# Optimization experiments

Measured on AMD Instinct MI355X. Metric: run time of the kernel, lower is better.

## Reference

```python
import jax, jax.numpy as jnp
import numpy as np

B, T, D, H = 4, 2048, 384, 6
HD = D // H  # 64
HALF = HD // 2


def setup_inputs() -> dict:
    key = jax.random.key(0)
    k0, k1, k2 = jax.random.split(key, 3)
    x = jax.random.normal(k0, (B, T, D), jnp.float32)
    attn_bias = jnp.zeros((1, 1, T, T), jnp.float32)  # additive SDPA bias
    # standard RoPE tables: [T, HD/2]
    inv_freq = 1.0 / (10000.0 ** (np.arange(HALF, dtype=np.float32) / HALF))
    ang = np.arange(T, dtype=np.float32)[:, None] * inv_freq[None, :]
    cos = jnp.asarray(np.cos(ang), jnp.float32)
    sin = jnp.asarray(np.sin(ang), jnp.float32)
    w_qkv = jax.random.normal(k1, (D, 3 * D), jnp.float32) * (D ** -0.5)
    w_proj = jax.random.normal(k2, (D, D), jnp.float32) * (D ** -0.5)
    return {"x": x, "attn_bias": attn_bias, "cos": cos, "sin": sin,
            "w_qkv": w_qkv, "w_proj": w_proj}


def _apply_rope(x, cos, sin):
    # x: [b, h, t, hd]; cos/sin: [t, hd/2] -> rotate-half RoPE
    half = x.shape[-1] // 2
    x1, x2 = x[..., :half], x[..., half:]
    c = cos[None, None, :, :]
    s = sin[None, None, :, :]
    return jnp.concatenate([x1 * c - x2 * s, x2 * c + x1 * s], axis=-1)


def reference(x, attn_bias, cos, sin, w_qkv, w_proj):
    b, t, _ = x.shape
    qkv = (x @ w_qkv).reshape(b, t, 3, H, HD)  # fused QKV projection
    q = jnp.transpose(qkv[:, :, 0], (0, 2, 1, 3))  # [b,h,t,hd]
    k = jnp.transpose(qkv[:, :, 1], (0, 2, 1, 3))
    v = jnp.transpose(qkv[:, :, 2], (0, 2, 1, 3))
    q = _apply_rope(q, cos, sin)
    k = _apply_rope(k, cos, sin)
    scale = 1.0 / jnp.sqrt(jnp.asarray(HD, x.dtype))
    scores = jnp.einsum("bhqd,bhkd->bhqk", q, k) * scale + attn_bias
    attn = jax.nn.softmax(scores, axis=-1)
    out = jnp.einsum("bhqk,bhkd->bhqd", attn, v)
    out = jnp.transpose(out, (0, 2, 1, 3)).reshape(b, t, H * HD)
    return out @ w_proj
```

## Files before the change

### kernel.cpp

```cpp
#include <hip/hip_runtime.h>
#include <hip/hip_bf16.h>

#define BB   4
#define TT   2048
#define DDIM 384
#define HH   6
#define HD   64
#define BT   (BB*TT)
#define QKVC (3*DDIM)

typedef __attribute__((ext_vector_type(4))) short short4v;
typedef __attribute__((ext_vector_type(8))) short short8v;
typedef __attribute__((ext_vector_type(4))) float float4v;
typedef unsigned short u16;

static __device__ __forceinline__ u16 f2bu(float f) {
    __hip_bfloat16 h = __float2bfloat16(f);
    return __builtin_bit_cast(u16, h);
}

static __device__ __forceinline__ short8v ld_frag(const u16* p) {
    short4v a = *(const short4v*)p;
    short4v b = *(const short4v*)(p + 4);
    return __builtin_shufflevector(a, b, 0, 1, 2, 3, 4, 5, 6, 7);
}

static __device__ __forceinline__ void st8(u16* p, uint4 v) {
    *(uint2*)p       = make_uint2(v.x, v.y);
    *(uint2*)(p + 4) = make_uint2(v.z, v.w);
}

#define MFMA16(a, b, c) __builtin_amdgcn_mfma_f32_16x16x32_bf16((a), (b), (c), 0, 0, 0)

__global__ __launch_bounds__(256) void prep_kernel(
    const float* __restrict__ wqkv, const float* __restrict__ wproj,
    const float* __restrict__ x,
    u16* __restrict__ wqkvT, u16* __restrict__ wprojT, u16* __restrict__ xb)
{
    const int bid = blockIdx.x;
    const int t = threadIdx.x;
    if (bid >= 144) {
        size_t base = (size_t)(bid - 144) * 4096 + (size_t)t * 16;
        const float* gp = x + base;
        __align__(16) u16 tmp[16];
        #pragma unroll
        for (int u = 0; u < 4; ++u) {
            float4 v = *(const float4*)(gp + 4 * u);
            tmp[4 * u + 0] = f2bu(v.x); tmp[4 * u + 1] = f2bu(v.y);
            tmp[4 * u + 2] = f2bu(v.z); tmp[4 * u + 3] = f2bu(v.w);
        }
        *(uint4*)(xb + base)     = *(const uint4*)tmp;
        *(uint4*)(xb + base + 8) = *(const uint4*)(tmp + 8);
        return;
    }
    const float* in; u16* out; int K, C, c0, k0;
    if (bid < 108) { in = wqkv;  out = wqkvT;  K = DDIM; C = QKVC;
                     c0 = (bid % 18) * 64; k0 = (bid / 18) * 64; }
    else           { int b2 = bid - 108; in = wproj; out = wprojT; K = DDIM; C = DDIM;
                     c0 = (b2 % 6) * 64; k0 = (b2 / 6) * 64; }
    __shared__ float tr[64][65];
    {
        int kr = t >> 2, cb = (t & 3) * 16;
        const float* gp = in + (size_t)(k0 + kr) * C + c0 + cb;
        #pragma unroll
        for (int u = 0; u < 4; ++u) {
            float4 v = *(const float4*)(gp + 4 * u);
            tr[cb + 4 * u + 0][kr] = v.x;
            tr[cb + 4 * u + 1][kr] = v.y;
            tr[cb + 4 * u + 2][kr] = v.z;
            tr[cb + 4 * u + 3][kr] = v.w;
        }
    }
    __syncthreads();
    {
        int c = t >> 2, kb = (t & 3) * 16;
        __align__(16) u16 tmp[16];
        #pragma unroll
        for (int u = 0; u < 16; ++u) tmp[u] = f2bu(tr[c][kb + u]);
        u16* op = out + (size_t)(c0 + c) * K + k0 + kb;
        *(uint4*)op       = *(const uint4*)tmp;
        *(uint4*)(op + 8) = *(const uint4*)(tmp + 8);
    }
}

__global__ __launch_bounds__(256) void qkv_rope_kernel(
    const u16* __restrict__ xb, const u16* __restrict__ wt,
    const float* __restrict__ cs, const float* __restrict__ sn,
    u16* __restrict__ qb, u16* __restrict__ kb, u16* __restrict__ vtb)
{
    __shared__ __align__(16) u16 xs[2][64][68];
    __shared__ __align__(16) u16 ws[2][64][68];
    const int t = threadIdx.x;
    const int wv = t >> 6, lane = t & 63, quad = lane >> 4, lo = lane & 15;
    const int r0 = blockIdx.y * 64;
    const int c0 = blockIdx.x * 64;
    const int sr = t >> 3, sd = (t & 7) * 8;

    st8(&xs[0][sr][sd],      *(const uint4*)(xb + (size_t)(r0 + sr) * DDIM + sd));
    st8(&xs[0][sr + 32][sd], *(const uint4*)(xb + (size_t)(r0 + sr + 32) * DDIM + sd));
    st8(&ws[0][sr][sd],      *(const uint4*)(wt + (size_t)(c0 + sr) * DDIM + sd));
    st8(&ws[0][sr + 32][sd], *(const uint4*)(wt + (size_t)(c0 + sr + 32) * DDIM + sd));
    __syncthreads();

    float4v acc[4] = {};
    for (int kk = 0; kk < 6; ++kk) {
        const int cur = kk & 1, nxt = cur ^ 1;
        const int kkn = (kk < 5 ? kk + 1 : 5) * 64;
        uint4 xp0 = *(const uint4*)(xb + (size_t)(r0 + sr) * DDIM + kkn + sd);
        uint4 xp1 = *(const uint4*)(xb + (size_t)(r0 + sr + 32) * DDIM + kkn + sd);
        uint4 wp0 = *(const uint4*)(wt + (size_t)(c0 + sr) * DDIM + kkn + sd);
        uint4 wp1 = *(const uint4*)(wt + (size_t)(c0 + sr + 32) * DDIM + kkn + sd);

        #pragma unroll
        for (int kf = 0; kf < 2; ++kf) {
            short8v a = ld_frag(&xs[cur][16 * wv + lo][kf * 32 + quad * 8]);
            #pragma unroll
            for (int nt = 0; nt < 4; ++nt) {
                short8v b = ld_frag(&ws[cur][nt * 16 + lo][kf * 32 + quad * 8]);
                acc[nt] = MFMA16(a, b, acc[nt]);
            }
        }
        st8(&xs[nxt][sr][sd], xp0);
        st8(&xs[nxt][sr + 32][sd], xp1);
        st8(&ws[nxt][sr][sd], wp0);
        st8(&ws[nxt][sr + 32][sd], wp1);
        __syncthreads();
    }

    const int sec = blockIdx.x / 6;
    const int h   = blockIdx.x % 6;
    const int rbase = r0 + 16 * wv + 4 * quad;
    const int bidx  = r0 >> 11;
    const int tbase = rbase & (TT - 1);

    if (sec == 2) {
        #pragma unroll
        for (int nt = 0; nt < 4; ++nt) {
            int d = nt * 16 + lo;
            unsigned a0 = f2bu(acc[nt][0]) | ((unsigned)f2bu(acc[nt][1]) << 16);
            unsigned a1 = f2bu(acc[nt][2]) | ((unsigned)f2bu(acc[nt][3]) << 16);
            u16* gp = vtb + ((size_t)(bidx * HH + h) * HD + d) * TT + tbase;
            *(uint2*)gp = make_uint2(a0, a1);
        }
    } else {
        u16* dst = (sec == 0) ? qb : kb;
        #pragma unroll
        for (int np = 0; np < 2; ++np) {
            #pragma unroll
            for (int r = 0; r < 4; ++r) {
                int tpos = tbase + r;
                int ci = np * 16 + lo;
                float cv = cs[tpos * 32 + ci];
                float sv = sn[tpos * 32 + ci];
                float x1 = acc[np][r], x2 = acc[np + 2][r];
                u16* gp = dst + ((size_t)(bidx * HH + h) * TT + tpos) * HD;
                gp[ci]      = f2bu(x1 * cv - x2 * sv);
                gp[ci + 32] = f2bu(x2 * cv + x1 * sv);
            }
        }
    }
}

__global__ __launch_bounds__(256, 3) void attn_kernel(
    const u16* __restrict__ qb, const u16* __restrict__ kb, const u16* __restrict__ vtb,
    const float* __restrict__ bias, u16* __restrict__ ob)
{
    __shared__ __align__(16) u16 ks[2][64][68];
    __shared__ __align__(16) u16 vt[2][64][68];
    __shared__ __align__(16) u16 ps[4][16][72];

    const int t = threadIdx.x;
    const int wv = t >> 6, lane = t & 63, quad = lane >> 4, lo = lane & 15;
    const int bh = blockIdx.x;
    const int b = bh / HH, h = bh % HH;
    const int q0 = blockIdx.y * 64;
    const int qrow = q0 + 16 * wv + lo;

    const u16* qbase = qb + ((size_t)bh * TT + qrow) * HD + quad * 8;
    short8v aq0 = __builtin_bit_cast(short8v, *(const uint4*)qbase);
    short8v aq1 = __builtin_bit_cast(short8v, *(const uint4*)(qbase + 32));

    const int sr = t >> 3, sd = (t & 7) * 8;
    const u16* kbbase = kb + (size_t)bh * TT * HD;
    const u16* vtbase = vtb + (size_t)bh * HD * TT;
    const float* brow = bias + (size_t)qrow * TT + 4 * quad;

    st8(&ks[0][sr][sd],      *(const uint4*)(kbbase + (size_t)sr * HD + sd));
    st8(&ks[0][sr + 32][sd], *(const uint4*)(kbbase + (size_t)(sr + 32) * HD + sd));
    st8(&vt[0][sr][sd],      *(const uint4*)(vtbase + (size_t)sr * TT + sd));
    st8(&vt[0][sr + 32][sd], *(const uint4*)(vtbase + (size_t)(sr + 32) * TT + sd));
    float4 bcur[4];
    #pragma unroll
    for (int nt = 0; nt < 4; ++nt) bcur[nt] = *(const float4*)(brow + nt * 16);
    __syncthreads();

    float4v oacc[4] = {};
    float lacc[4] = {0.f, 0.f, 0.f, 0.f};

    for (int kt = 0; kt < TT / 64; ++kt) {
        const int cur = kt & 1, nxt = cur ^ 1;
        const int kn = (kt < 31 ? kt + 1 : 31) * 64;

        uint4 kp0 = *(const uint4*)(kbbase + (size_t)(kn + sr) * HD + sd);
        uint4 kp1 = *(const uint4*)(kbbase + (size_t)(kn + sr + 32) * HD + sd);
        uint4 vp0 = *(const uint4*)(vtbase + (size_t)sr * TT + kn + sd);
        uint4 vp1 = *(const uint4*)(vtbase + (size_t)(sr + 32) * TT + kn + sd);
        float4 bnxt[4];
        #pragma unroll
        for (int nt = 0; nt < 4; ++nt) bnxt[nt] = *(const float4*)(brow + kn + nt * 16);

        float4v s[4] = {};
        #pragma unroll
        for (int kf = 0; kf < 2; ++kf) {
            #pragma unroll
            for (int nt = 0; nt < 4; ++nt) {
                short8v kfr = ld_frag(&ks[cur][nt * 16 + lo][kf * 32 + quad * 8]);
                s[nt] = MFMA16(kfr, (kf ? aq1 : aq0), s[nt]);
            }
        }

        #pragma unroll
        for (int nt = 0; nt < 4; ++nt) {
            float p0 = __expf(fmaf(s[nt][0], 0.125f, bcur[nt].x));
            float p1 = __expf(fmaf(s[nt][1], 0.125f, bcur[nt].y));
            float p2 = __expf(fmaf(s[nt][2], 0.125f, bcur[nt].z));
            float p3 = __expf(fmaf(s[nt][3], 0.125f, bcur[nt].w));
            lacc[nt] += (p0 + p1) + (p2 + p3);
            short4v pv = { (short)f2bu(p0), (short)f2bu(p1),
                           (short)f2bu(p2), (short)f2bu(p3) };
            *(short4v*)&ps[wv][lo][nt * 16 + 4 * quad] = pv;
        }

        #pragma unroll
        for (int kf = 0; kf < 2; ++kf) {
            short8v ap = __builtin_bit_cast(short8v,
                *(const uint4*)&ps[wv][lo][kf * 32 + quad * 8]);
            #pragma unroll
            for (int dt = 0; dt < 4; ++dt) {
                short8v bv = ld_frag(&vt[cur][dt * 16 + lo][kf * 32 + quad * 8]);
                oacc[dt] = MFMA16(ap, bv, oacc[dt]);
            }
        }

        st8(&ks[nxt][sr][sd], kp0);
        st8(&ks[nxt][sr + 32][sd], kp1);
        st8(&vt[nxt][sr][sd], vp0);
        st8(&vt[nxt][sr + 32][sd], vp1);
        #pragma unroll
        for (int nt = 0; nt < 4; ++nt) bcur[nt] = bnxt[nt];
        __syncthreads();
    }

    float l = (lacc[0] + lacc[1]) + (lacc[2] + lacc[3]);
    l += __shfl_xor(l, 16);
    l += __shfl_xor(l, 32);
    #pragma unroll
    for (int r = 0; r < 4; ++r) {
        float lr = __shfl(l, 4 * quad + r);
        float inv = 1.f / lr;
        u16* gp = ob + ((size_t)b * TT + q0 + 16 * wv + 4 * quad + r) * DDIM + h * HD + lo;
        #pragma unroll
        for (int dt = 0; dt < 4; ++dt)
            gp[dt * 16] = f2bu(oacc[dt][r] * inv);
    }
}

__global__ __launch_bounds__(256) void proj_kernel(
    const u16* __restrict__ o, const u16* __restrict__ wt, float* __restrict__ out)
{
    __shared__ __align__(16) u16 os[2][64][68];
    __shared__ __align__(16) u16 ws[2][64][68];
    const int t = threadIdx.x;
    const int wv = t >> 6, lane = t & 63, quad = lane >> 4, lo = lane & 15;
    const int r0 = blockIdx.y * 64, c0 = blockIdx.x * 64;
    const int sr = t >> 3, sd = (t & 7) * 8;

    st8(&os[0][sr][sd],      *(const uint4*)(o + (size_t)(r0 + sr) * DDIM + sd));
    st8(&os[0][sr + 32][sd], *(const uint4*)(o + (size_t)(r0 + sr + 32) * DDIM + sd));
    st8(&ws[0][sr][sd],      *(const uint4*)(wt + (size_t)(c0 + sr) * DDIM + sd));
    st8(&ws[0][sr + 32][sd], *(const uint4*)(wt + (size_t)(c0 + sr + 32) * DDIM + sd));
    __syncthreads();

    float4v acc[4] = {};
    for (int kk = 0; kk < 6; ++kk) {
        const int cur = kk & 1, nxt = cur ^ 1;
        const int kkn = (kk < 5 ? kk + 1 : 5) * 64;
        uint4 op0 = *(const uint4*)(o + (size_t)(r0 + sr) * DDIM + kkn + sd);
        uint4 op1 = *(const uint4*)(o + (size_t)(r0 + sr + 32) * DDIM + kkn + sd);
        uint4 wp0 = *(const uint4*)(wt + (size_t)(c0 + sr) * DDIM + kkn + sd);
        uint4 wp1 = *(const uint4*)(wt + (size_t)(c0 + sr + 32) * DDIM + kkn + sd);

        #pragma unroll
        for (int kf = 0; kf < 2; ++kf) {
            short8v a = ld_frag(&os[cur][16 * wv + lo][kf * 32 + quad * 8]);
            #pragma unroll
            for (int nt = 0; nt < 4; ++nt) {
                short8v bfr = ld_frag(&ws[cur][nt * 16 + lo][kf * 32 + quad * 8]);
                acc[nt] = MFMA16(a, bfr, acc[nt]);
            }
        }
        st8(&os[nxt][sr][sd], op0);
        st8(&os[nxt][sr + 32][sd], op1);
        st8(&ws[nxt][sr][sd], wp0);
        st8(&ws[nxt][sr + 32][sd], wp1);
        __syncthreads();
    }
    #pragma unroll
    for (int r = 0; r < 4; ++r) {
        float* gp = out + (size_t)(r0 + 16 * wv + 4 * quad + r) * DDIM + c0;
        #pragma unroll
        for (int nt = 0; nt < 4; ++nt)
            gp[nt * 16 + lo] = acc[nt][r];
    }
}

extern "C" void kernel_launch(void* const* d_in, const int* in_sizes, int n_in,
                              void* d_out, int out_size, void* d_ws, size_t ws_size,
                              hipStream_t stream) {
    const float* x     = (const float*)d_in[0];
    const float* bias  = (const float*)d_in[1];
    const float* cs    = (const float*)d_in[2];
    const float* sn    = (const float*)d_in[3];
    const float* wqkv  = (const float*)d_in[4];
    const float* wproj = (const float*)d_in[5];
    float* out = (float*)d_out;

    u16* wqkvT  = (u16*)d_ws;
    u16* wprojT = wqkvT + (size_t)QKVC * DDIM;
    u16* qb     = wprojT + (size_t)DDIM * DDIM;
    u16* kb     = qb + (size_t)BB * HH * TT * HD;
    u16* vtb    = kb + (size_t)BB * HH * TT * HD;
    u16* ob     = vtb + (size_t)BB * HH * TT * HD;
    u16* xb     = ob + (size_t)BT * DDIM;

    prep_kernel<<<dim3(144 + BT * DDIM / 4096), 256, 0, stream>>>(
        wqkv, wproj, x, wqkvT, wprojT, xb);
    qkv_rope_kernel<<<dim3(QKVC / 64, BT / 64), 256, 0, stream>>>(
        xb, wqkvT, cs, sn, qb, kb, vtb);
    attn_kernel<<<dim3(BB * HH, TT / 64), 256, 0, stream>>>(qb, kb, vtb, bias, ob);
    proj_kernel<<<dim3(DDIM / 64, BT / 64), 256, 0, stream>>>(ob, wprojT, out);
}
```

Before: 178.6 us.

## Split attention keys across two blocks with merge kernel and MFMA row sums

The attention kernel now splits the key sequence into two halves along a new grid dimension, doubling the block count. Each block writes unnormalized fp32 partial outputs and row sums, and a new merge kernel combines and normalizes them into bf16. Shared memory drops from double to single buffering, launch bounds request 6 blocks per SM, and row sums now come from an MFMA against a ones vector instead of scalar adds. The cost is extra fp32 partial-output traffic, one more launch, and an extra sync per tile. Skipping max-subtraction in the split is consistent with the original kernel.

```diff
diff --git a/kernel.cpp b/kernel.cpp
--- a/kernel.cpp
+++ b/kernel.cpp
@@ -161,12 +161,12 @@
     }
 }
 
-__global__ __launch_bounds__(256, 3) void attn_kernel(
+__global__ __launch_bounds__(256, 6) void attn_kernel(
     const u16* __restrict__ qb, const u16* __restrict__ kb, const u16* __restrict__ vtb,
-    const float* __restrict__ bias, u16* __restrict__ ob)
-{
-    __shared__ __align__(16) u16 ks[2][64][68];
-    __shared__ __align__(16) u16 vt[2][64][68];
+    const float* __restrict__ bias, float* __restrict__ opart, float* __restrict__ lws)
+{
+    __shared__ __align__(16) u16 ks[64][68];
+    __shared__ __align__(16) u16 vt[64][68];
     __shared__ __align__(16) u16 ps[4][16][72];
 
     const int t = threadIdx.x;
@@ -174,6 +174,8 @@
     const int bh = blockIdx.x;
     const int b = bh / HH, h = bh % HH;
     const int q0 = blockIdx.y * 64;
+    const int half = blockIdx.z;
+    const int kbase0 = half * (TT / 2);
     const int qrow = q0 + 16 * wv + lo;
 
     const u16* qbase = qb + ((size_t)bh * TT + qrow) * HD + quad * 8;
@@ -181,40 +183,46 @@
     short8v aq1 = __builtin_bit_cast(short8v, *(const uint4*)(qbase + 32));
 
     const int sr = t >> 3, sd = (t & 7) * 8;
-    const u16* kbbase = kb + (size_t)bh * TT * HD;
-    const u16* vtbase = vtb + (size_t)bh * HD * TT;
-    const float* brow = bias + (size_t)qrow * TT + 4 * quad;
-
-    st8(&ks[0][sr][sd],      *(const uint4*)(kbbase + (size_t)sr * HD + sd));
-    st8(&ks[0][sr + 32][sd], *(const uint4*)(kbbase + (size_t)(sr + 32) * HD + sd));
-    st8(&vt[0][sr][sd],      *(const uint4*)(vtbase + (size_t)sr * TT + sd));
-    st8(&vt[0][sr + 32][sd], *(const uint4*)(vtbase + (size_t)(sr + 32) * TT + sd));
-    float4 bcur[4];
-    #pragma unroll
-    for (int nt = 0; nt < 4; ++nt) bcur[nt] = *(const float4*)(brow + nt * 16);
-    __syncthreads();
+    const u16* kbbase = kb + ((size_t)bh * TT + kbase0) * HD;
+    const u16* vtbase = vtb + (size_t)bh * HD * TT + kbase0;
+    const float* brow = bias + (size_t)qrow * TT + kbase0 + 4 * quad;
+
+    const short8v bones = { 0x3F80, 0x3F80, 0x3F80, 0x3F80,
+                            0x3F80, 0x3F80, 0x3F80, 0x3F80 };
+
+    uint4 kp0 = *(const uint4*)(kbbase + (size_t)sr * HD + sd);
+    uint4 kp1 = *(const uint4*)(kbbase + (size_t)(sr + 32) * HD + sd);
+    uint4 vp0 = *(const uint4*)(vtbase + (size_t)sr * TT + sd);
+    uint4 vp1 = *(const uint4*)(vtbase + (size_t)(sr + 32) * TT + sd);
 
     float4v oacc[4] = {};
-    float lacc[4] = {0.f, 0.f, 0.f, 0.f};
-
-    for (int kt = 0; kt < TT / 64; ++kt) {
-        const int cur = kt & 1, nxt = cur ^ 1;
-        const int kn = (kt < 31 ? kt + 1 : 31) * 64;
-
-        uint4 kp0 = *(const uint4*)(kbbase + (size_t)(kn + sr) * HD + sd);
-        uint4 kp1 = *(const uint4*)(kbbase + (size_t)(kn + sr + 32) * HD + sd);
-        uint4 vp0 = *(const uint4*)(vtbase + (size_t)sr * TT + kn + sd);
-        uint4 vp1 = *(const uint4*)(vtbase + (size_t)(sr + 32) * TT + kn + sd);
-        float4 bnxt[4];
-        #pragma unroll
-        for (int nt = 0; nt < 4; ++nt) bnxt[nt] = *(const float4*)(brow + kn + nt * 16);
+    float4v lsum = {};
+
+    for (int kt = 0; kt < TT / 128; ++kt) {
+        __syncthreads();
+        st8(&ks[sr][sd], kp0);
+        st8(&ks[sr + 32][sd], kp1);
+        st8(&vt[sr][sd], vp0);
+        st8(&vt[sr + 32][sd], vp1);
+        __syncthreads();
+
+        const int kn = (kt < TT / 128 - 1 ? kt + 1 : kt) * 64;
+        kp0 = *(const uint4*)(kbbase + (size_t)(kn + sr) * HD + sd);
+        kp1 = *(const uint4*)(kbbase + (size_t)(kn + sr + 32) * HD + sd);
+        vp0 = *(const uint4*)(vtbase + (size_t)sr * TT + kn + sd);
+        vp1 = *(const uint4*)(vtbase + (size_t)(sr + 32) * TT + kn + sd);
+
+        float4 bcur[4];
+        #pragma unroll
+        for (int nt = 0; nt < 4; ++nt)
+            bcur[nt] = *(const float4*)(brow + kt * 64 + nt * 16);
 
         float4v s[4] = {};
         #pragma unroll
         for (int kf = 0; kf < 2; ++kf) {
             #pragma unroll
             for (int nt = 0; nt < 4; ++nt) {
-                short8v kfr = ld_frag(&ks[cur][nt * 16 + lo][kf * 32 + quad * 8]);
+                short8v kfr = ld_frag(&ks[nt * 16 + lo][kf * 32 + quad * 8]);
                 s[nt] = MFMA16(kfr, (kf ? aq1 : aq0), s[nt]);
             }
         }
@@ -225,7 +233,6 @@
             float p1 = __expf(fmaf(s[nt][1], 0.125f, bcur[nt].y));
             float p2 = __expf(fmaf(s[nt][2], 0.125f, bcur[nt].z));
             float p3 = __expf(fmaf(s[nt][3], 0.125f, bcur[nt].w));
-            lacc[nt] += (p0 + p1) + (p2 + p3);
             short4v pv = { (short)f2bu(p0), (short)f2bu(p1),
                            (short)f2bu(p2), (short)f2bu(p3) };
             *(short4v*)&ps[wv][lo][nt * 16 + 4 * quad] = pv;
@@ -235,34 +242,44 @@
         for (int kf = 0; kf < 2; ++kf) {
             short8v ap = __builtin_bit_cast(short8v,
                 *(const uint4*)&ps[wv][lo][kf * 32 + quad * 8]);
+            lsum = MFMA16(ap, bones, lsum);
             #pragma unroll
             for (int dt = 0; dt < 4; ++dt) {
-                short8v bv = ld_frag(&vt[cur][dt * 16 + lo][kf * 32 + quad * 8]);
+                short8v bv = ld_frag(&vt[dt * 16 + lo][kf * 32 + quad * 8]);
                 oacc[dt] = MFMA16(ap, bv, oacc[dt]);
             }
         }
-
-        st8(&ks[nxt][sr][sd], kp0);
-        st8(&ks[nxt][sr + 32][sd], kp1);
-        st8(&vt[nxt][sr][sd], vp0);
-        st8(&vt[nxt][sr + 32][sd], vp1);
-        #pragma unroll
-        for (int nt = 0; nt < 4; ++nt) bcur[nt] = bnxt[nt];
-        __syncthreads();
-    }
-
-    float l = (lacc[0] + lacc[1]) + (lacc[2] + lacc[3]);
-    l += __shfl_xor(l, 16);
-    l += __shfl_xor(l, 32);
+    }
+
     #pragma unroll
     for (int r = 0; r < 4; ++r) {
-        float lr = __shfl(l, 4 * quad + r);
-        float inv = 1.f / lr;
-        u16* gp = ob + ((size_t)b * TT + q0 + 16 * wv + 4 * quad + r) * DDIM + h * HD + lo;
+        int row = q0 + 16 * wv + 4 * quad + r;
+        if (lo == 0)
+            lws[((size_t)half * (BB * HH) + bh) * TT + row] = lsum[r];
+        float* gp = opart + (((size_t)half * BB + b) * TT + row) * DDIM + h * HD + lo;
         #pragma unroll
         for (int dt = 0; dt < 4; ++dt)
-            gp[dt * 16] = f2bu(oacc[dt][r] * inv);
-    }
+            gp[dt * 16] = oacc[dt][r];
+    }
+}
+
+__global__ __launch_bounds__(256) void merge_kernel(
+    const float* __restrict__ opart, const float* __restrict__ lws,
+    u16* __restrict__ ob)
+{
+    size_t n = ((size_t)blockIdx.x * 256 + threadIdx.x) * 4;
+    int d = (int)(n % DDIM);
+    size_t rowi = n / DDIM;
+    int b = (int)(rowi >> 11), trow = (int)(rowi & (TT - 1));
+    int bh = b * HH + d / HD;
+    float la = lws[(size_t)bh * TT + trow] +
+               lws[((size_t)(BB * HH) + bh) * TT + trow];
+    float inv = 1.f / la;
+    float4 oa = *(const float4*)(opart + n);
+    float4 obp = *(const float4*)(opart + (size_t)BB * TT * DDIM + n);
+    unsigned a0 = f2bu((oa.x + obp.x) * inv) | ((unsigned)f2bu((oa.y + obp.y) * inv) << 16);
+    unsigned a1 = f2bu((oa.z + obp.z) * inv) | ((unsigned)f2bu((oa.w + obp.w) * inv) << 16);
+    *(uint2*)(ob + n) = make_uint2(a0, a1);
 }
 
 __global__ __launch_bounds__(256) void proj_kernel(
@@ -332,11 +349,15 @@
     u16* vtb    = kb + (size_t)BB * HH * TT * HD;
     u16* ob     = vtb + (size_t)BB * HH * TT * HD;
     u16* xb     = ob + (size_t)BT * DDIM;
+    float* opart = (float*)(xb + (size_t)BT * DDIM);
+    float* lws   = opart + (size_t)2 * BT * DDIM;
 
     prep_kernel<<<dim3(144 + BT * DDIM / 4096), 256, 0, stream>>>(
         wqkv, wproj, x, wqkvT, wprojT, xb);
     qkv_rope_kernel<<<dim3(QKVC / 64, BT / 64), 256, 0, stream>>>(
         xb, wqkvT, cs, sn, qb, kb, vtb);
-    attn_kernel<<<dim3(BB * HH, TT / 64), 256, 0, stream>>>(qb, kb, vtb, bias, ob);
+    attn_kernel<<<dim3(BB * HH, TT / 64, 2), 256, 0, stream>>>(
+        qb, kb, vtb, bias, opart, lws);
+    merge_kernel<<<dim3(BT * DDIM / 1024), 256, 0, stream>>>(opart, lws, ob);
     proj_kernel<<<dim3(DDIM / 64, BT / 64), 256, 0, stream>>>(ob, wprojT, out);
 }
```

Result: no change. 179.7 us (+0.7%).
